# Kernel optimization log

Measured on AMD Instinct MI355X. Metric: run time of the kernel, lower is better.

## Reference

```python
import jax, jax.numpy as jnp
import numpy as np

N = 50000      # nodes
E = 800000     # edges
IN = 128       # in_channels
HID = 64       # hidden_channels per head
HEADS = 2
OUT = 64       # out_channels of second conv
ED = 16        # edge_dim
NEG = 0.2      # LeakyReLU negative slope (PyG default)


def setup_inputs() -> dict:
    key = jax.random.key(0)
    ks = jax.random.split(key, 24)
    def p(k, shape, scale=0.05):
        return jax.random.normal(k, shape, jnp.float32) * scale
    inp = {}
    inp["x"] = jax.random.normal(ks[0], (N, IN), jnp.float32)
    inp["edge_index"] = jax.random.randint(ks[1], (2, E), 0, N, jnp.int32)
    inp["edge_attr"] = jax.random.normal(ks[2], (E, ED), jnp.float32)
    # GATv2Conv layer 1 (heads=HEADS, out=HID)
    inp["Wl1"] = p(ks[3], (IN, HEADS * HID)); inp["bl1"] = jnp.zeros((HEADS * HID,), jnp.float32)
    inp["Wr1"] = p(ks[4], (IN, HEADS * HID)); inp["br1"] = jnp.zeros((HEADS * HID,), jnp.float32)
    inp["We1"] = p(ks[5], (ED, HEADS * HID))
    inp["att1"] = p(ks[6], (HEADS, HID))
    inp["b1"] = jnp.zeros((HEADS * HID,), jnp.float32)
    # GATv2Conv layer 2 (heads=1, out=OUT), input dim = HEADS*HID
    inp["Wl2"] = p(ks[7], (HEADS * HID, OUT)); inp["bl2"] = jnp.zeros((OUT,), jnp.float32)
    inp["Wr2"] = p(ks[8], (HEADS * HID, OUT)); inp["br2"] = jnp.zeros((OUT,), jnp.float32)
    inp["We2"] = p(ks[9], (ED, OUT))
    inp["att2"] = p(ks[10], (1, OUT))
    inp["b2"] = jnp.zeros((OUT,), jnp.float32)
    # edge MLP: Linear(2*OUT, OUT) -> ReLU -> Linear(OUT, 1)
    inp["Wm1"] = p(ks[11], (2 * OUT, OUT)); inp["bm1"] = jnp.zeros((OUT,), jnp.float32)
    inp["Wm2"] = p(ks[12], (OUT, 1)); inp["bm2"] = jnp.zeros((1,), jnp.float32)
    return inp


def add_self_loops(src, dst, edge_attr, n):
    # PyG add_self_loops with fill_value='mean': loop attr = mean of incoming edge attrs
    cnt = jax.ops.segment_sum(jnp.ones((src.shape[0],), edge_attr.dtype), dst, num_segments=n)
    loop_attr = jax.ops.segment_sum(edge_attr, dst, num_segments=n) / jnp.maximum(cnt, 1.0)[:, None]
    ar = jnp.arange(n, dtype=src.dtype)
    return (jnp.concatenate([src, ar]), jnp.concatenate([dst, ar]),
            jnp.concatenate([edge_attr, loop_attr], axis=0))


def gatv2_layer(x, src, dst, edge_attr, Wl, bl, Wr, br, We, att, bias, heads, out_ch):
    n = x.shape[0]
    xl = (x @ Wl + bl).reshape(n, heads, out_ch)   # messages (source side)
    xr = (x @ Wr + br).reshape(n, heads, out_ch)   # target side
    ea = (edge_attr @ We).reshape(-1, heads, out_ch)
    m = jax.nn.leaky_relu(xl[src] + xr[dst] + ea, NEG)      # [Et, H, C]
    logits = jnp.einsum('ehc,hc->eh', m, att)               # [Et, H]
    # segment softmax over destination node (every node has a self loop)
    mx = jax.ops.segment_max(logits, dst, num_segments=n)
    ex = jnp.exp(logits - mx[dst])
    den = jax.ops.segment_sum(ex, dst, num_segments=n)
    alpha = ex / den[dst]                                   # [Et, H]
    out = jax.ops.segment_sum(alpha[:, :, None] * xl[src], dst, num_segments=n)
    return out.reshape(n, heads * out_ch) + bias


def reference(x, edge_index, edge_attr,
              Wl1, bl1, Wr1, br1, We1, att1, b1,
              Wl2, bl2, Wr2, br2, We2, att2, b2,
              Wm1, bm1, Wm2, bm2):
    src, dst = edge_index[0], edge_index[1]
    n = x.shape[0]
    s2, d2, ea2 = add_self_loops(src, dst, edge_attr, n)
    h = gatv2_layer(x, s2, d2, ea2, Wl1, bl1, Wr1, br1, We1, att1, b1, HEADS, HID)
    h = jax.nn.elu(h)
    h = gatv2_layer(h, s2, d2, ea2, Wl2, bl2, Wr2, br2, We2, att2, b2, 1, OUT)
    # edge predictor over the ORIGINAL edges
    ei = jnp.concatenate([h[src], h[dst]], axis=1)          # [E, 2*OUT]
    z = jax.nn.relu(ei @ Wm1 + bm1)
    return z @ Wm2 + bm2                                    # [E, 1]
```

## Files before the change

### kernel.cpp

```cpp
#include <hip/hip_runtime.h>
#include <cstdint>
#include <cstddef>


__device__ __forceinline__ float half_sum(float v) {
#pragma unroll
  for (int o = 1; o <= 16; o <<= 1) v += __shfl_xor(v, o, 64);
  return v;
}

__global__ __launch_bounds__(256) void cnt_kernel(const int* __restrict__ dst,
                                                  int* __restrict__ cnt, int E) {
  int e = blockIdx.x * 256 + threadIdx.x;
  if (e < E) atomicAdd(&cnt[dst[e]], 1);
}

__global__ __launch_bounds__(256) void scan_blocksum_kernel(
    const int* __restrict__ cnt, int* __restrict__ partial, int Nn) {
  int i = blockIdx.x * 256 + threadIdx.x;
  int v = (i < Nn) ? cnt[i] : 0;
#pragma unroll
  for (int o = 32; o > 0; o >>= 1) v += __shfl_xor(v, o, 64);
  __shared__ int ws[4];
  if ((threadIdx.x & 63) == 0) ws[threadIdx.x >> 6] = v;
  __syncthreads();
  if (threadIdx.x == 0) partial[blockIdx.x] = ws[0] + ws[1] + ws[2] + ws[3];
}

__global__ __launch_bounds__(256) void scan_partial_kernel(
    int* __restrict__ partial, int* __restrict__ rowptr, int nb, int Nn, int E) {
  __shared__ int buf[256];
  int t = threadIdx.x;
  int v = (t < nb) ? partial[t] : 0;
  buf[t] = v;
  __syncthreads();
  for (int o = 1; o < 256; o <<= 1) {
    int u = (t >= o) ? buf[t - o] : 0;
    __syncthreads();
    buf[t] += u;
    __syncthreads();
  }
  partial[t] = (t == 0) ? 0 : buf[t - 1];
  if (t == 0) rowptr[Nn] = E;
}

__global__ __launch_bounds__(256) void scan_write_kernel(
    const int* __restrict__ cnt, const int* __restrict__ partial,
    int* __restrict__ rowptr, int* __restrict__ cursor, int Nn) {
  __shared__ int buf[256];
  int i = blockIdx.x * 256 + threadIdx.x;
  int t = threadIdx.x;
  int v = (i < Nn) ? cnt[i] : 0;
  buf[t] = v;
  __syncthreads();
  for (int o = 1; o < 256; o <<= 1) {
    int u = (t >= o) ? buf[t - o] : 0;
    __syncthreads();
    buf[t] += u;
    __syncthreads();
  }
  if (i < Nn) {
    int r = partial[blockIdx.x] + buf[t] - v;
    rowptr[i] = r;
    cursor[i] = r;
  }
}

__global__ __launch_bounds__(256) void csr_build_kernel(
    const int* __restrict__ src, const int* __restrict__ dst,
    int* __restrict__ cursor, int2* __restrict__ es, int E) {
  int e = blockIdx.x * 256 + threadIdx.x;
  if (e >= E) return;
  int s = src[e], d = dst[e];
  int pos = atomicAdd(&cursor[d], 1);
  es[pos] = make_int2(e, s);
}

template <int K, int NC>
__global__ __launch_bounds__(256, 4) void gemm2_kernel(
    const float* __restrict__ A, const float* __restrict__ W1,
    const float* __restrict__ b1, float* __restrict__ C1,
    const float* __restrict__ W2, const float* __restrict__ b2,
    float* __restrict__ C2, int M) {
  const int BM = 64;
  const int CQ = NC / 4;
  const int RP = BM / (256 / CQ);
  __shared__ float Alds[BM * K];
  int row0 = blockIdx.x * BM;
  for (int i = threadIdx.x; i < BM * K / 4; i += 256) {
    int r = i / (K / 4);
    float4 v = make_float4(0.f, 0.f, 0.f, 0.f);
    if (row0 + r < M) v = ((const float4*)A)[(size_t)(row0 + r) * (K / 4) + (i % (K / 4))];
    ((float4*)Alds)[i] = v;
  }
  __syncthreads();
  int cq = threadIdx.x % CQ;
  int rg = threadIdx.x / CQ;
  float4 acc1[RP], acc2[RP];
#pragma unroll
  for (int r = 0; r < RP; r++) {
    acc1[r] = make_float4(0.f, 0.f, 0.f, 0.f);
    acc2[r] = make_float4(0.f, 0.f, 0.f, 0.f);
  }
  const float4* W14 = (const float4*)W1;
  const float4* W24 = (const float4*)W2;
  for (int k = 0; k < K; k += 4) {
    float4 u0 = W14[(size_t)(k + 0) * CQ + cq];
    float4 u1 = W14[(size_t)(k + 1) * CQ + cq];
    float4 u2 = W14[(size_t)(k + 2) * CQ + cq];
    float4 u3 = W14[(size_t)(k + 3) * CQ + cq];
    float4 v0 = W24[(size_t)(k + 0) * CQ + cq];
    float4 v1 = W24[(size_t)(k + 1) * CQ + cq];
    float4 v2 = W24[(size_t)(k + 2) * CQ + cq];
    float4 v3 = W24[(size_t)(k + 3) * CQ + cq];
#pragma unroll
    for (int r = 0; r < RP; r++) {
      float4 a = ((const float4*)Alds)[(rg * RP + r) * (K / 4) + (k >> 2)];
      acc1[r].x = fmaf(a.x, u0.x, acc1[r].x);
      acc1[r].y = fmaf(a.x, u0.y, acc1[r].y);
      acc1[r].z = fmaf(a.x, u0.z, acc1[r].z);
      acc1[r].w = fmaf(a.x, u0.w, acc1[r].w);
      acc1[r].x = fmaf(a.y, u1.x, acc1[r].x);
      acc1[r].y = fmaf(a.y, u1.y, acc1[r].y);
      acc1[r].z = fmaf(a.y, u1.z, acc1[r].z);
      acc1[r].w = fmaf(a.y, u1.w, acc1[r].w);
      acc1[r].x = fmaf(a.z, u2.x, acc1[r].x);
      acc1[r].y = fmaf(a.z, u2.y, acc1[r].y);
      acc1[r].z = fmaf(a.z, u2.z, acc1[r].z);
      acc1[r].w = fmaf(a.z, u2.w, acc1[r].w);
      acc1[r].x = fmaf(a.w, u3.x, acc1[r].x);
      acc1[r].y = fmaf(a.w, u3.y, acc1[r].y);
      acc1[r].z = fmaf(a.w, u3.z, acc1[r].z);
      acc1[r].w = fmaf(a.w, u3.w, acc1[r].w);
      acc2[r].x = fmaf(a.x, v0.x, acc2[r].x);
      acc2[r].y = fmaf(a.x, v0.y, acc2[r].y);
      acc2[r].z = fmaf(a.x, v0.z, acc2[r].z);
      acc2[r].w = fmaf(a.x, v0.w, acc2[r].w);
      acc2[r].x = fmaf(a.y, v1.x, acc2[r].x);
      acc2[r].y = fmaf(a.y, v1.y, acc2[r].y);
      acc2[r].z = fmaf(a.y, v1.z, acc2[r].z);
      acc2[r].w = fmaf(a.y, v1.w, acc2[r].w);
      acc2[r].x = fmaf(a.z, v2.x, acc2[r].x);
      acc2[r].y = fmaf(a.z, v2.y, acc2[r].y);
      acc2[r].z = fmaf(a.z, v2.z, acc2[r].z);
      acc2[r].w = fmaf(a.z, v2.w, acc2[r].w);
      acc2[r].x = fmaf(a.w, v3.x, acc2[r].x);
      acc2[r].y = fmaf(a.w, v3.y, acc2[r].y);
      acc2[r].z = fmaf(a.w, v3.z, acc2[r].z);
      acc2[r].w = fmaf(a.w, v3.w, acc2[r].w);
    }
  }
  float4 bb1 = b1 ? ((const float4*)b1)[cq] : make_float4(0.f, 0.f, 0.f, 0.f);
  float4 bb2 = b2 ? ((const float4*)b2)[cq] : make_float4(0.f, 0.f, 0.f, 0.f);
#pragma unroll
  for (int r = 0; r < RP; r++) {
    int row = row0 + rg * RP + r;
    if (row < M) {
      ((float4*)C1)[(size_t)row * CQ + cq] =
          make_float4(acc1[r].x + bb1.x, acc1[r].y + bb1.y, acc1[r].z + bb1.z,
                      acc1[r].w + bb1.w);
      ((float4*)C2)[(size_t)row * CQ + cq] =
          make_float4(acc2[r].x + bb2.x, acc2[r].y + bb2.y, acc2[r].z + bb2.z,
                      acc2[r].w + bb2.w);
    }
  }
}

template <int ELU>
__global__ __launch_bounds__(256, 4) void node_fused2_kernel(
    const int* __restrict__ rowptr, const int2* __restrict__ es,
    const float* __restrict__ edge_attr, const float* __restrict__ We,
    const float* __restrict__ att, const float* __restrict__ xl,
    const float* __restrict__ xr, const float* __restrict__ bias,
    float* __restrict__ out, int Nn) {
  int wid = blockIdx.x * 4 + (threadIdx.x >> 6);
  if (wid >= Nn) return;
  int l = threadIdx.x & 63;
  int ch = ((l >> 5) << 6) | ((l & 31) << 1);
  float2 we[16];
#pragma unroll
  for (int k = 0; k < 16; k++) we[k] = *(const float2*)(We + k * 128 + ch);
  float2 xr2 = *(const float2*)(xr + (size_t)wid * 128 + ch);
  float2 at2 = *(const float2*)(att + ch);
  int start = __builtin_amdgcn_readfirstlane(rowptr[wid]);
  int end = __builtin_amdgcn_readfirstlane(rowptr[wid + 1]);
  float m = -1e30f, sden = 0.f, accx = 0.f, accy = 0.f;
  float sax = 0.f, say = 0.f;
  if (end > start) {
    float4 A0, A1, A2, A3;
    float2 X;
    int2 en;
    {
      int2 ec = es[start];
      const float4* p4 = (const float4*)(edge_attr + (size_t)ec.x * 16);
      A0 = p4[0]; A1 = p4[1]; A2 = p4[2]; A3 = p4[3];
      X = *(const float2*)(xl + (size_t)ec.y * 128 + ch);
      en = es[min(start + 1, end - 1)];
    }
    for (int j = start; j < end; ++j) {
      int2 e2 = es[min(j + 2, end - 1)];
      const float4* p4 = (const float4*)(edge_attr + (size_t)en.x * 16);
      float4 B0 = p4[0], B1 = p4[1], B2 = p4[2], B3 = p4[3];
      float2 Y = *(const float2*)(xl + (size_t)en.y * 128 + ch);
      float av[16] = {A0.x, A0.y, A0.z, A0.w, A1.x, A1.y, A1.z, A1.w,
                      A2.x, A2.y, A2.z, A2.w, A3.x, A3.y, A3.z, A3.w};
      float ex = 0.f, ey = 0.f;
#pragma unroll
      for (int k = 0; k < 16; k++) {
        ex = fmaf(av[k], we[k].x, ex);
        ey = fmaf(av[k], we[k].y, ey);
      }
      sax += ex;
      say += ey;
      float mx = X.x + xr2.x + ex;
      float my = X.y + xr2.y + ey;
      mx = (mx >= 0.f) ? mx : 0.2f * mx;
      my = (my >= 0.f) ? my : 0.2f * my;
      float p = half_sum(fmaf(at2.x, mx, at2.y * my));
      float nm = fmaxf(m, p);
      float r = __expf(m - nm), ep = __expf(p - nm);
      sden = fmaf(sden, r, ep);
      accx = fmaf(accx, r, ep * X.x);
      accy = fmaf(accy, r, ep * X.y);
      m = nm;
      A0 = B0; A1 = B1; A2 = B2; A3 = B3; X = Y;
      en = e2;
    }
  }
  {
    float denom = 1.f / fmaxf((float)(end - start), 1.f);
    float2 Xs = *(const float2*)(xl + (size_t)wid * 128 + ch);
    float mx = Xs.x + xr2.x + sax * denom;
    float my = Xs.y + xr2.y + say * denom;
    mx = (mx >= 0.f) ? mx : 0.2f * mx;
    my = (my >= 0.f) ? my : 0.2f * my;
    float p = half_sum(fmaf(at2.x, mx, at2.y * my));
    float nm = fmaxf(m, p);
    float r = __expf(m - nm), ep = __expf(p - nm);
    sden = fmaf(sden, r, ep);
    accx = fmaf(accx, r, ep * Xs.x);
    accy = fmaf(accy, r, ep * Xs.y);
  }
  float inv = 1.f / sden;
  float2 b2 = *(const float2*)(bias + ch);
  float vx = fmaf(accx, inv, b2.x);
  float vy = fmaf(accy, inv, b2.y);
  if (ELU) {
    vx = (vx > 0.f) ? vx : expm1f(vx);
    vy = (vy > 0.f) ? vy : expm1f(vy);
  }
  *(float2*)(out + (size_t)wid * 128 + ch) = make_float2(vx, vy);
}

__global__ __launch_bounds__(256, 4) void node_fused1_kernel(
    const int* __restrict__ rowptr, const int2* __restrict__ es,
    const float* __restrict__ edge_attr, const float* __restrict__ We,
    const float* __restrict__ att, const float* __restrict__ xl,
    const float* __restrict__ xr, const float* __restrict__ bias,
    float* __restrict__ out, int Nn) {
  int wid = blockIdx.x * 4 + (threadIdx.x >> 6);
  if (wid >= Nn) return;
  int l = threadIdx.x & 63;
  int half = l >> 5;
  int ch = (l & 31) << 1;
  float2 we[16];
#pragma unroll
  for (int k = 0; k < 16; k++) we[k] = *(const float2*)(We + k * 64 + ch);
  float2 xr2 = *(const float2*)(xr + (size_t)wid * 64 + ch);
  float2 at2 = *(const float2*)(att + ch);
  int start = __builtin_amdgcn_readfirstlane(rowptr[wid]);
  int end = __builtin_amdgcn_readfirstlane(rowptr[wid + 1]);
  float m = -1e30f, sden = 0.f, accx = 0.f, accy = 0.f;
  float sax = 0.f, say = 0.f;
  if (end > start) {
    float4 A0, A1, A2, A3;
    float2 X;
    int2 en;
    {
      int jc = min(start + half, end - 1);
      int2 ec = es[jc];
      const float4* p4 = (const float4*)(edge_attr + (size_t)ec.x * 16);
      A0 = p4[0]; A1 = p4[1]; A2 = p4[2]; A3 = p4[3];
      X = *(const float2*)(xl + (size_t)ec.y * 64 + ch);
      en = es[min(start + 2 + half, end - 1)];
    }
    for (int j = start; j < end; j += 2) {
      int2 e2 = es[min(j + 4 + half, end - 1)];
      const float4* p4 = (const float4*)(edge_attr + (size_t)en.x * 16);
      float4 B0 = p4[0], B1 = p4[1], B2 = p4[2], B3 = p4[3];
      float2 Y = *(const float2*)(xl + (size_t)en.y * 64 + ch);
      float av[16] = {A0.x, A0.y, A0.z, A0.w, A1.x, A1.y, A1.z, A1.w,
                      A2.x, A2.y, A2.z, A2.w, A3.x, A3.y, A3.z, A3.w};
      float ex = 0.f, ey = 0.f;
#pragma unroll
      for (int k = 0; k < 16; k++) {
        ex = fmaf(av[k], we[k].x, ex);
        ey = fmaf(av[k], we[k].y, ey);
      }
      bool dead = (j + half) >= end;
      sax += dead ? 0.f : ex;
      say += dead ? 0.f : ey;
      float mx = X.x + xr2.x + ex;
      float my = X.y + xr2.y + ey;
      mx = (mx >= 0.f) ? mx : 0.2f * mx;
      my = (my >= 0.f) ? my : 0.2f * my;
      float p = half_sum(fmaf(at2.x, mx, at2.y * my));
      p = dead ? -1e30f : p;
      float nm = fmaxf(m, p);
      float r = __expf(m - nm), ep = __expf(p - nm);
      ep = dead ? 0.f : ep;
      sden = fmaf(sden, r, ep);
      accx = fmaf(accx, r, ep * X.x);
      accy = fmaf(accy, r, ep * X.y);
      m = nm;
      A0 = B0; A1 = B1; A2 = B2; A3 = B3; X = Y;
      en = e2;
    }
  }
  float mo = __shfl_xor(m, 32, 64);
  float so = __shfl_xor(sden, 32, 64);
  float aox = __shfl_xor(accx, 32, 64);
  float aoy = __shfl_xor(accy, 32, 64);
  float M = fmaxf(m, mo);
  float ra = __expf(m - M), rb = __expf(mo - M);
  float S = fmaf(sden, ra, so * rb);
  float AX = fmaf(accx, ra, aox * rb);
  float AY = fmaf(accy, ra, aoy * rb);
  float saxt = sax + __shfl_xor(sax, 32, 64);
  float sayt = say + __shfl_xor(say, 32, 64);
  {
    float denom = 1.f / fmaxf((float)(end - start), 1.f);
    float2 Xs = *(const float2*)(xl + (size_t)wid * 64 + ch);
    float mx = Xs.x + xr2.x + saxt * denom;
    float my = Xs.y + xr2.y + sayt * denom;
    mx = (mx >= 0.f) ? mx : 0.2f * mx;
    my = (my >= 0.f) ? my : 0.2f * my;
    float p = half_sum(fmaf(at2.x, mx, at2.y * my));
    float nm = fmaxf(M, p);
    float r = __expf(M - nm), ep = __expf(p - nm);
    S = fmaf(S, r, ep);
    AX = fmaf(AX, r, ep * Xs.x);
    AY = fmaf(AY, r, ep * Xs.y);
  }
  if (half == 0) {
    float inv = 1.f / S;
    float2 b2 = *(const float2*)(bias + ch);
    *(float2*)(out + (size_t)wid * 64 + ch) =
        make_float2(fmaf(AX, inv, b2.x), fmaf(AY, inv, b2.y));
  }
}

__global__ __launch_bounds__(256) void edge_mlp_kernel(
    const int* __restrict__ src, const int* __restrict__ dst,
    const float* __restrict__ aa, const float* __restrict__ bb,
    const float* __restrict__ Wm2, const float* __restrict__ bm2,
    float* __restrict__ out, int E) {
  int t = blockIdx.x * 256 + threadIdx.x;
  int eid = t >> 4;
  if (eid >= E) return;
  int g = threadIdx.x & 15;
  float4 w = ((const float4*)Wm2)[g];
  int s = src[eid], d = dst[eid];
  float4 za = ((const float4*)aa)[(size_t)s * 16 + g];
  float4 zb = ((const float4*)bb)[(size_t)d * 16 + g];
  float p = fmaxf(za.x + zb.x, 0.f) * w.x;
  p = fmaf(fmaxf(za.y + zb.y, 0.f), w.y, p);
  p = fmaf(fmaxf(za.z + zb.z, 0.f), w.z, p);
  p = fmaf(fmaxf(za.w + zb.w, 0.f), w.w, p);
#pragma unroll
  for (int o = 8; o > 0; o >>= 1) p += __shfl_xor(p, o, 64);
  if (g == 0) out[eid] = p + bm2[0];
}

extern "C" void kernel_launch(void* const* d_in, const int* in_sizes, int n_in,
                              void* d_out, int out_size, void* d_ws,
                              size_t ws_size, hipStream_t stream) {
  const float* x = (const float*)d_in[0];
  const int* ei = (const int*)d_in[1];
  const float* edge_attr = (const float*)d_in[2];
  const float* Wl1 = (const float*)d_in[3];
  const float* bl1 = (const float*)d_in[4];
  const float* Wr1 = (const float*)d_in[5];
  const float* br1 = (const float*)d_in[6];
  const float* We1 = (const float*)d_in[7];
  const float* att1 = (const float*)d_in[8];
  const float* b1 = (const float*)d_in[9];
  const float* Wl2 = (const float*)d_in[10];
  const float* bl2 = (const float*)d_in[11];
  const float* Wr2 = (const float*)d_in[12];
  const float* br2 = (const float*)d_in[13];
  const float* We2 = (const float*)d_in[14];
  const float* att2 = (const float*)d_in[15];
  const float* b2 = (const float*)d_in[16];
  const float* Wm1 = (const float*)d_in[17];
  const float* bm1 = (const float*)d_in[18];
  const float* Wm2 = (const float*)d_in[19];
  const float* bm2 = (const float*)d_in[20];

  const int Nn = in_sizes[0] / 128;
  const int E = in_sizes[1] / 2;
  const int* src = ei;
  const int* dst = ei + E;
  const int nb = (Nn + 255) / 256;

  char* ws = (char*)d_ws;
  size_t off = 0;
  auto alloc = [&](size_t bytes) -> char* {
    char* p = ws + off;
    off += (bytes + 255) & ~(size_t)255;
    return p;
  };
  int* cnt = (int*)alloc((size_t)Nn * 4);
  int* rowptr = (int*)alloc((size_t)(Nn + 1) * 4);
  int* cursor = (int*)alloc((size_t)Nn * 4);
  int* partial = (int*)alloc(256 * 4);
  int2* es = (int2*)alloc((size_t)E * 8);
  float* xl = (float*)alloc((size_t)Nn * 128 * 4);
  float* xr = (float*)alloc((size_t)Nn * 128 * 4);
  float* h1 = (float*)alloc((size_t)Nn * 128 * 4);
  float* h2 = (float*)alloc((size_t)Nn * 64 * 4);
  float* aa = xl;
  float* bb = xr;

  hipMemsetAsync(cnt, 0, (size_t)Nn * 4, stream);

  cnt_kernel<<<(E + 255) / 256, 256, 0, stream>>>(dst, cnt, E);
  scan_blocksum_kernel<<<nb, 256, 0, stream>>>(cnt, partial, Nn);
  scan_partial_kernel<<<1, 256, 0, stream>>>(partial, rowptr, nb, Nn, E);
  scan_write_kernel<<<nb, 256, 0, stream>>>(cnt, partial, rowptr, cursor, Nn);
  csr_build_kernel<<<(E + 255) / 256, 256, 0, stream>>>(src, dst, cursor, es, E);

  gemm2_kernel<128, 128><<<(Nn + 63) / 64, 256, 0, stream>>>(
      x, Wl1, bl1, xl, Wr1, br1, xr, Nn);
  node_fused2_kernel<1><<<(Nn + 3) / 4, 256, 0, stream>>>(
      rowptr, es, edge_attr, We1, att1, xl, xr, b1, h1, Nn);

  gemm2_kernel<128, 64><<<(Nn + 63) / 64, 256, 0, stream>>>(
      h1, Wl2, bl2, xl, Wr2, br2, xr, Nn);
  node_fused1_kernel<<<(Nn + 3) / 4, 256, 0, stream>>>(
      rowptr, es, edge_attr, We2, att2, xl, xr, b2, h2, Nn);

  gemm2_kernel<64, 64><<<(Nn + 63) / 64, 256, 0, stream>>>(
      h2, Wm1, nullptr, aa, Wm1 + 64 * 64, bm1, bb, Nn);
  edge_mlp_kernel<<<(E * 16 + 255) / 256, 256, 0, stream>>>(src, dst, aa, bb,
                                                            Wm2, bm2,
                                                            (float*)d_out, E);
}
```

Baseline: 676.8 us.

## Pre-sort edge attributes into CSR order and process four edges per iteration

The CSR build now emits a separate source permutation and an edge-position map, and a new scatter kernel copies edge_attr into destination-sorted order so both node kernels read edge features contiguously rather than gathering them. Both aggregation kernels process four edges per loop step with batched shuffle reductions and one online-softmax update per group, and keep the edge weight matrix in LDS instead of registers. The layer-2 kernel goes from two half-waves splitting edges to one channel per lane with a full-wave reduction. The cost is an extra scatter pass over the edge attributes and more workspace memory.

After: 671.5 us. No clear change (-0.8%).

```diff
diff --git a/kernel.cpp b/kernel.cpp
--- a/kernel.cpp
+++ b/kernel.cpp
@@ -2,12 +2,6 @@
 #include <cstdint>
 #include <cstddef>
 
-
-__device__ __forceinline__ float half_sum(float v) {
-#pragma unroll
-  for (int o = 1; o <= 16; o <<= 1) v += __shfl_xor(v, o, 64);
-  return v;
-}
 
 __global__ __launch_bounds__(256) void cnt_kernel(const int* __restrict__ dst,
                                                   int* __restrict__ cnt, int E) {
@@ -68,12 +62,23 @@
 
 __global__ __launch_bounds__(256) void csr_build_kernel(
     const int* __restrict__ src, const int* __restrict__ dst,
-    int* __restrict__ cursor, int2* __restrict__ es, int E) {
+    int* __restrict__ cursor, int* __restrict__ sperm, int* __restrict__ pperm,
+    int E) {
   int e = blockIdx.x * 256 + threadIdx.x;
   if (e >= E) return;
   int s = src[e], d = dst[e];
   int pos = atomicAdd(&cursor[d], 1);
-  es[pos] = make_int2(e, s);
+  sperm[pos] = s;
+  pperm[e] = pos;
+}
+
+__global__ __launch_bounds__(256) void ea_scatter_kernel(
+    const float* __restrict__ edge_attr, const int* __restrict__ pperm,
+    float* __restrict__ ea_sorted, int E) {
+  int t = blockIdx.x * 256 + threadIdx.x;
+  if (t >= E * 16) return;
+  int e = t >> 4, k = t & 15;
+  ea_sorted[(size_t)pperm[e] * 16 + k] = edge_attr[t];
 }
 
 template <int K, int NC>
@@ -167,65 +172,84 @@
 }
 
 template <int ELU>
-__global__ __launch_bounds__(256, 4) void node_fused2_kernel(
-    const int* __restrict__ rowptr, const int2* __restrict__ es,
-    const float* __restrict__ edge_attr, const float* __restrict__ We,
+__global__ __launch_bounds__(256) void node_fused2_kernel(
+    const int* __restrict__ rowptr, const int* __restrict__ sperm,
+    const float* __restrict__ ea_sorted, const float* __restrict__ We,
     const float* __restrict__ att, const float* __restrict__ xl,
     const float* __restrict__ xr, const float* __restrict__ bias,
     float* __restrict__ out, int Nn) {
+  __shared__ float weLds[16 * 128];
+  for (int i = threadIdx.x; i < 16 * 128 / 4; i += 256)
+    ((float4*)weLds)[i] = ((const float4*)We)[i];
+  __syncthreads();
   int wid = blockIdx.x * 4 + (threadIdx.x >> 6);
   if (wid >= Nn) return;
   int l = threadIdx.x & 63;
   int ch = ((l >> 5) << 6) | ((l & 31) << 1);
-  float2 we[16];
-#pragma unroll
-  for (int k = 0; k < 16; k++) we[k] = *(const float2*)(We + k * 128 + ch);
+  const float* wp = weLds + ch;
   float2 xr2 = *(const float2*)(xr + (size_t)wid * 128 + ch);
   float2 at2 = *(const float2*)(att + ch);
   int start = __builtin_amdgcn_readfirstlane(rowptr[wid]);
   int end = __builtin_amdgcn_readfirstlane(rowptr[wid + 1]);
   float m = -1e30f, sden = 0.f, accx = 0.f, accy = 0.f;
   float sax = 0.f, say = 0.f;
-  if (end > start) {
-    float4 A0, A1, A2, A3;
-    float2 X;
-    int2 en;
-    {
-      int2 ec = es[start];
-      const float4* p4 = (const float4*)(edge_attr + (size_t)ec.x * 16);
-      A0 = p4[0]; A1 = p4[1]; A2 = p4[2]; A3 = p4[3];
-      X = *(const float2*)(xl + (size_t)ec.y * 128 + ch);
-      en = es[min(start + 1, end - 1)];
-    }
-    for (int j = start; j < end; ++j) {
-      int2 e2 = es[min(j + 2, end - 1)];
-      const float4* p4 = (const float4*)(edge_attr + (size_t)en.x * 16);
-      float4 B0 = p4[0], B1 = p4[1], B2 = p4[2], B3 = p4[3];
-      float2 Y = *(const float2*)(xl + (size_t)en.y * 128 + ch);
-      float av[16] = {A0.x, A0.y, A0.z, A0.w, A1.x, A1.y, A1.z, A1.w,
-                      A2.x, A2.y, A2.z, A2.w, A3.x, A3.y, A3.z, A3.w};
-      float ex = 0.f, ey = 0.f;
-#pragma unroll
-      for (int k = 0; k < 16; k++) {
-        ex = fmaf(av[k], we[k].x, ex);
-        ey = fmaf(av[k], we[k].y, ey);
-      }
-      sax += ex;
-      say += ey;
-      float mx = X.x + xr2.x + ex;
-      float my = X.y + xr2.y + ey;
-      mx = (mx >= 0.f) ? mx : 0.2f * mx;
-      my = (my >= 0.f) ? my : 0.2f * my;
-      float p = half_sum(fmaf(at2.x, mx, at2.y * my));
-      float nm = fmaxf(m, p);
-      float r = __expf(m - nm), ep = __expf(p - nm);
-      sden = fmaf(sden, r, ep);
-      accx = fmaf(accx, r, ep * X.x);
-      accy = fmaf(accy, r, ep * X.y);
-      m = nm;
-      A0 = B0; A1 = B1; A2 = B2; A3 = B3; X = Y;
-      en = e2;
-    }
+  for (int j = start; j < end; j += 4) {
+    bool f1 = (j + 1 < end), f2 = (j + 2 < end), f3 = (j + 3 < end);
+    int j1 = f1 ? j + 1 : j, j2 = f2 ? j + 2 : j, j3 = f3 ? j + 3 : j;
+    int s0 = sperm[j], s1 = sperm[j1], s2 = sperm[j2], s3 = sperm[j3];
+    float2 X0 = *(const float2*)(xl + (size_t)s0 * 128 + ch);
+    float2 X1 = *(const float2*)(xl + (size_t)s1 * 128 + ch);
+    float2 X2 = *(const float2*)(xl + (size_t)s2 * 128 + ch);
+    float2 X3 = *(const float2*)(xl + (size_t)s3 * 128 + ch);
+    const float* e0p = ea_sorted + (size_t)j * 16;
+    const float* e1p = ea_sorted + (size_t)j1 * 16;
+    const float* e2p = ea_sorted + (size_t)j2 * 16;
+    const float* e3p = ea_sorted + (size_t)j3 * 16;
+    float ex0 = 0.f, ey0 = 0.f, ex1 = 0.f, ey1 = 0.f;
+    float ex2 = 0.f, ey2 = 0.f, ex3 = 0.f, ey3 = 0.f;
+#pragma unroll
+    for (int k = 0; k < 16; k++) {
+      float2 w = *(const float2*)(wp + k * 128);
+      float a0 = e0p[k], a1 = e1p[k], a2 = e2p[k], a3 = e3p[k];
+      ex0 = fmaf(a0, w.x, ex0); ey0 = fmaf(a0, w.y, ey0);
+      ex1 = fmaf(a1, w.x, ex1); ey1 = fmaf(a1, w.y, ey1);
+      ex2 = fmaf(a2, w.x, ex2); ey2 = fmaf(a2, w.y, ey2);
+      ex3 = fmaf(a3, w.x, ex3); ey3 = fmaf(a3, w.y, ey3);
+    }
+    float mx, my;
+    mx = X0.x + xr2.x + ex0; my = X0.y + xr2.y + ey0;
+    mx = (mx >= 0.f) ? mx : 0.2f * mx; my = (my >= 0.f) ? my : 0.2f * my;
+    float p0 = fmaf(at2.x, mx, at2.y * my);
+    mx = X1.x + xr2.x + ex1; my = X1.y + xr2.y + ey1;
+    mx = (mx >= 0.f) ? mx : 0.2f * mx; my = (my >= 0.f) ? my : 0.2f * my;
+    float p1 = fmaf(at2.x, mx, at2.y * my);
+    mx = X2.x + xr2.x + ex2; my = X2.y + xr2.y + ey2;
+    mx = (mx >= 0.f) ? mx : 0.2f * mx; my = (my >= 0.f) ? my : 0.2f * my;
+    float p2 = fmaf(at2.x, mx, at2.y * my);
+    mx = X3.x + xr2.x + ex3; my = X3.y + xr2.y + ey3;
+    mx = (mx >= 0.f) ? mx : 0.2f * mx; my = (my >= 0.f) ? my : 0.2f * my;
+    float p3 = fmaf(at2.x, mx, at2.y * my);
+#pragma unroll
+    for (int o = 1; o <= 16; o <<= 1) {
+      p0 += __shfl_xor(p0, o, 64);
+      p1 += __shfl_xor(p1, o, 64);
+      p2 += __shfl_xor(p2, o, 64);
+      p3 += __shfl_xor(p3, o, 64);
+    }
+    p1 = f1 ? p1 : -1e30f;
+    p2 = f2 ? p2 : -1e30f;
+    p3 = f3 ? p3 : -1e30f;
+    float pm = fmaxf(fmaxf(p0, p1), fmaxf(p2, p3));
+    float nm = fmaxf(m, pm);
+    float r = __expf(m - nm);
+    float q0 = __expf(p0 - nm), q1 = __expf(p1 - nm);
+    float q2 = __expf(p2 - nm), q3 = __expf(p3 - nm);
+    sden = fmaf(sden, r, (q0 + q1) + (q2 + q3));
+    accx = fmaf(accx, r, fmaf(q0, X0.x, q1 * X1.x) + fmaf(q2, X2.x, q3 * X3.x));
+    accy = fmaf(accy, r, fmaf(q0, X0.y, q1 * X1.y) + fmaf(q2, X2.y, q3 * X3.y));
+    m = nm;
+    sax += ex0 + (f1 ? ex1 : 0.f) + (f2 ? ex2 : 0.f) + (f3 ? ex3 : 0.f);
+    say += ey0 + (f1 ? ey1 : 0.f) + (f2 ? ey2 : 0.f) + (f3 ? ey3 : 0.f);
   }
   {
     float denom = 1.f / fmaxf((float)(end - start), 1.f);
@@ -234,7 +258,9 @@
     float my = Xs.y + xr2.y + say * denom;
     mx = (mx >= 0.f) ? mx : 0.2f * mx;
     my = (my >= 0.f) ? my : 0.2f * my;
-    float p = half_sum(fmaf(at2.x, mx, at2.y * my));
+    float p = fmaf(at2.x, mx, at2.y * my);
+#pragma unroll
+    for (int o = 1; o <= 16; o <<= 1) p += __shfl_xor(p, o, 64);
     float nm = fmaxf(m, p);
     float r = __expf(m - nm), ep = __expf(p - nm);
     sden = fmaf(sden, r, ep);
@@ -252,102 +278,85 @@
   *(float2*)(out + (size_t)wid * 128 + ch) = make_float2(vx, vy);
 }
 
-__global__ __launch_bounds__(256, 4) void node_fused1_kernel(
-    const int* __restrict__ rowptr, const int2* __restrict__ es,
-    const float* __restrict__ edge_attr, const float* __restrict__ We,
+__global__ __launch_bounds__(256) void node_fused1_kernel(
+    const int* __restrict__ rowptr, const int* __restrict__ sperm,
+    const float* __restrict__ ea_sorted, const float* __restrict__ We,
     const float* __restrict__ att, const float* __restrict__ xl,
     const float* __restrict__ xr, const float* __restrict__ bias,
     float* __restrict__ out, int Nn) {
+  __shared__ float weLds[16 * 64];
+  if (threadIdx.x < 256)
+    ((float4*)weLds)[threadIdx.x] = ((const float4*)We)[threadIdx.x];
+  __syncthreads();
   int wid = blockIdx.x * 4 + (threadIdx.x >> 6);
   if (wid >= Nn) return;
   int l = threadIdx.x & 63;
-  int half = l >> 5;
-  int ch = (l & 31) << 1;
-  float2 we[16];
-#pragma unroll
-  for (int k = 0; k < 16; k++) we[k] = *(const float2*)(We + k * 64 + ch);
-  float2 xr2 = *(const float2*)(xr + (size_t)wid * 64 + ch);
-  float2 at2 = *(const float2*)(att + ch);
+  const float* wp = weLds + l;
+  float xr1 = xr[(size_t)wid * 64 + l];
+  float a1 = att[l];
   int start = __builtin_amdgcn_readfirstlane(rowptr[wid]);
   int end = __builtin_amdgcn_readfirstlane(rowptr[wid + 1]);
-  float m = -1e30f, sden = 0.f, accx = 0.f, accy = 0.f;
-  float sax = 0.f, say = 0.f;
-  if (end > start) {
-    float4 A0, A1, A2, A3;
-    float2 X;
-    int2 en;
-    {
-      int jc = min(start + half, end - 1);
-      int2 ec = es[jc];
-      const float4* p4 = (const float4*)(edge_attr + (size_t)ec.x * 16);
-      A0 = p4[0]; A1 = p4[1]; A2 = p4[2]; A3 = p4[3];
-      X = *(const float2*)(xl + (size_t)ec.y * 64 + ch);
-      en = es[min(start + 2 + half, end - 1)];
-    }
-    for (int j = start; j < end; j += 2) {
-      int2 e2 = es[min(j + 4 + half, end - 1)];
-      const float4* p4 = (const float4*)(edge_attr + (size_t)en.x * 16);
-      float4 B0 = p4[0], B1 = p4[1], B2 = p4[2], B3 = p4[3];
-      float2 Y = *(const float2*)(xl + (size_t)en.y * 64 + ch);
-      float av[16] = {A0.x, A0.y, A0.z, A0.w, A1.x, A1.y, A1.z, A1.w,
-                      A2.x, A2.y, A2.z, A2.w, A3.x, A3.y, A3.z, A3.w};
-      float ex = 0.f, ey = 0.f;
-#pragma unroll
-      for (int k = 0; k < 16; k++) {
-        ex = fmaf(av[k], we[k].x, ex);
-        ey = fmaf(av[k], we[k].y, ey);
-      }
-      bool dead = (j + half) >= end;
-      sax += dead ? 0.f : ex;
-      say += dead ? 0.f : ey;
-      float mx = X.x + xr2.x + ex;
-      float my = X.y + xr2.y + ey;
-      mx = (mx >= 0.f) ? mx : 0.2f * mx;
-      my = (my >= 0.f) ? my : 0.2f * my;
-      float p = half_sum(fmaf(at2.x, mx, at2.y * my));
-      p = dead ? -1e30f : p;
-      float nm = fmaxf(m, p);
-      float r = __expf(m - nm), ep = __expf(p - nm);
-      ep = dead ? 0.f : ep;
-      sden = fmaf(sden, r, ep);
-      accx = fmaf(accx, r, ep * X.x);
-      accy = fmaf(accy, r, ep * X.y);
-      m = nm;
-      A0 = B0; A1 = B1; A2 = B2; A3 = B3; X = Y;
-      en = e2;
-    }
-  }
-  float mo = __shfl_xor(m, 32, 64);
-  float so = __shfl_xor(sden, 32, 64);
-  float aox = __shfl_xor(accx, 32, 64);
-  float aoy = __shfl_xor(accy, 32, 64);
-  float M = fmaxf(m, mo);
-  float ra = __expf(m - M), rb = __expf(mo - M);
-  float S = fmaf(sden, ra, so * rb);
-  float AX = fmaf(accx, ra, aox * rb);
-  float AY = fmaf(accy, ra, aoy * rb);
-  float saxt = sax + __shfl_xor(sax, 32, 64);
-  float sayt = say + __shfl_xor(say, 32, 64);
+  float m = -1e30f, sden = 0.f, acc = 0.f, sa = 0.f;
+  for (int j = start; j < end; j += 4) {
+    bool f1 = (j + 1 < end), f2 = (j + 2 < end), f3 = (j + 3 < end);
+    int j1 = f1 ? j + 1 : j, j2 = f2 ? j + 2 : j, j3 = f3 ? j + 3 : j;
+    int s0 = sperm[j], s1 = sperm[j1], s2 = sperm[j2], s3 = sperm[j3];
+    float X0 = xl[(size_t)s0 * 64 + l];
+    float X1 = xl[(size_t)s1 * 64 + l];
+    float X2 = xl[(size_t)s2 * 64 + l];
+    float X3 = xl[(size_t)s3 * 64 + l];
+    const float* e0p = ea_sorted + (size_t)j * 16;
+    const float* e1p = ea_sorted + (size_t)j1 * 16;
+    const float* e2p = ea_sorted + (size_t)j2 * 16;
+    const float* e3p = ea_sorted + (size_t)j3 * 16;
+    float ex0 = 0.f, ex1 = 0.f, ex2 = 0.f, ex3 = 0.f;
+#pragma unroll
+    for (int k = 0; k < 16; k++) {
+      float w = wp[k * 64];
+      ex0 = fmaf(e0p[k], w, ex0);
+      ex1 = fmaf(e1p[k], w, ex1);
+      ex2 = fmaf(e2p[k], w, ex2);
+      ex3 = fmaf(e3p[k], w, ex3);
+    }
+    float t;
+    t = X0 + xr1 + ex0; t = (t >= 0.f) ? t : 0.2f * t; float p0 = a1 * t;
+    t = X1 + xr1 + ex1; t = (t >= 0.f) ? t : 0.2f * t; float p1 = a1 * t;
+    t = X2 + xr1 + ex2; t = (t >= 0.f) ? t : 0.2f * t; float p2 = a1 * t;
+    t = X3 + xr1 + ex3; t = (t >= 0.f) ? t : 0.2f * t; float p3 = a1 * t;
+#pragma unroll
+    for (int o = 1; o <= 32; o <<= 1) {
+      p0 += __shfl_xor(p0, o, 64);
+      p1 += __shfl_xor(p1, o, 64);
+      p2 += __shfl_xor(p2, o, 64);
+      p3 += __shfl_xor(p3, o, 64);
+    }
+    p1 = f1 ? p1 : -1e30f;
+    p2 = f2 ? p2 : -1e30f;
+    p3 = f3 ? p3 : -1e30f;
+    float pm = fmaxf(fmaxf(p0, p1), fmaxf(p2, p3));
+    float nm = fmaxf(m, pm);
+    float r = __expf(m - nm);
+    float q0 = __expf(p0 - nm), q1 = __expf(p1 - nm);
+    float q2 = __expf(p2 - nm), q3 = __expf(p3 - nm);
+    sden = fmaf(sden, r, (q0 + q1) + (q2 + q3));
+    acc = fmaf(acc, r, fmaf(q0, X0, q1 * X1) + fmaf(q2, X2, q3 * X3));
+    m = nm;
+    sa += ex0 + (f1 ? ex1 : 0.f) + (f2 ? ex2 : 0.f) + (f3 ? ex3 : 0.f);
+  }
   {
     float denom = 1.f / fmaxf((float)(end - start), 1.f);
-    float2 Xs = *(const float2*)(xl + (size_t)wid * 64 + ch);
-    float mx = Xs.x + xr2.x + saxt * denom;
-    float my = Xs.y + xr2.y + sayt * denom;
-    mx = (mx >= 0.f) ? mx : 0.2f * mx;
-    my = (my >= 0.f) ? my : 0.2f * my;
-    float p = half_sum(fmaf(at2.x, mx, at2.y * my));
-    float nm = fmaxf(M, p);
-    float r = __expf(M - nm), ep = __expf(p - nm);
-    S = fmaf(S, r, ep);
-    AX = fmaf(AX, r, ep * Xs.x);
-    AY = fmaf(AY, r, ep * Xs.y);
-  }
-  if (half == 0) {
-    float inv = 1.f / S;
-    float2 b2 = *(const float2*)(bias + ch);
-    *(float2*)(out + (size_t)wid * 64 + ch) =
-        make_float2(fmaf(AX, inv, b2.x), fmaf(AY, inv, b2.y));
-  }
+    float Xs = xl[(size_t)wid * 64 + l];
+    float t = Xs + xr1 + sa * denom;
+    t = (t >= 0.f) ? t : 0.2f * t;
+    float p = a1 * t;
+#pragma unroll
+    for (int o = 1; o <= 32; o <<= 1) p += __shfl_xor(p, o, 64);
+    float nm = fmaxf(m, p);
+    float r = __expf(m - nm), ep = __expf(p - nm);
+    sden = fmaf(sden, r, ep);
+    acc = fmaf(acc, r, ep * Xs);
+  }
+  out[(size_t)wid * 64 + l] = fmaf(acc, 1.f / sden, bias[l]);
 }
 
 __global__ __launch_bounds__(256) void edge_mlp_kernel(
@@ -414,7 +423,9 @@
   int* rowptr = (int*)alloc((size_t)(Nn + 1) * 4);
   int* cursor = (int*)alloc((size_t)Nn * 4);
   int* partial = (int*)alloc(256 * 4);
-  int2* es = (int2*)alloc((size_t)E * 8);
+  int* sperm = (int*)alloc((size_t)E * 4);
+  int* pperm = (int*)alloc((size_t)E * 4);
+  float* ea_sorted = (float*)alloc((size_t)E * 16 * 4);
   float* xl = (float*)alloc((size_t)Nn * 128 * 4);
   float* xr = (float*)alloc((size_t)Nn * 128 * 4);
   float* h1 = (float*)alloc((size_t)Nn * 128 * 4);
@@ -428,17 +439,20 @@
   scan_blocksum_kernel<<<nb, 256, 0, stream>>>(cnt, partial, Nn);
   scan_partial_kernel<<<1, 256, 0, stream>>>(partial, rowptr, nb, Nn, E);
   scan_write_kernel<<<nb, 256, 0, stream>>>(cnt, partial, rowptr, cursor, Nn);
-  csr_build_kernel<<<(E + 255) / 256, 256, 0, stream>>>(src, dst, cursor, es, E);
+  csr_build_kernel<<<(E + 255) / 256, 256, 0, stream>>>(src, dst, cursor, sperm,
+                                                        pperm, E);
+  ea_scatter_kernel<<<(E * 16 + 255) / 256, 256, 0, stream>>>(edge_attr, pperm,
+                                                              ea_sorted, E);
 
   gemm2_kernel<128, 128><<<(Nn + 63) / 64, 256, 0, stream>>>(
       x, Wl1, bl1, xl, Wr1, br1, xr, Nn);
   node_fused2_kernel<1><<<(Nn + 3) / 4, 256, 0, stream>>>(
-      rowptr, es, edge_attr, We1, att1, xl, xr, b1, h1, Nn);
+      rowptr, sperm, ea_sorted, We1, att1, xl, xr, b1, h1, Nn);
 
   gemm2_kernel<128, 64><<<(Nn + 63) / 64, 256, 0, stream>>>(
       h1, Wl2, bl2, xl, Wr2, br2, xr, Nn);
   node_fused1_kernel<<<(Nn + 3) / 4, 256, 0, stream>>>(
-      rowptr, es, edge_attr, We2, att2, xl, xr, b2, h2, Nn);
+      rowptr, sperm, ea_sorted, We2, att2, xl, xr, b2, h2, Nn);
 
   gemm2_kernel<64, 64><<<(Nn + 63) / 64, 256, 0, stream>>>(
       h2, Wm1, nullptr, aa, Wm1 + 64 * 64, bm1, bb, Nn);
```
